# Kernel optimization log

Hardware: AMD Instinct MI355X
Metric: run time of the kernel (lower is better)

The kernel has to match this reference:

```python
import jax, jax.numpy as jnp
import numpy as np

DIM = 3072
HEADS = 24
HD = 128
FF = 4 * DIM
EPS = 1e-6
SCALE_SHIFT = 1.0


def _ln(x):
    # LayerNorm, elementwise_affine=False
    mu = jnp.mean(x, axis=-1, keepdims=True)
    var = jnp.mean(jnp.square(x - mu), axis=-1, keepdims=True)
    return (x - mu) * jax.lax.rsqrt(var + EPS)


def _rms(x, w):
    # RMSNorm over head_dim with learned weight
    ms = jnp.mean(jnp.square(x), axis=-1, keepdims=True)
    return x * jax.lax.rsqrt(ms + EPS) * w


def _rope(x, cos, sin):
    # x: [B,S,H,D], cos/sin: [S,D]; interleaved rotate-half (diffusers style)
    xr = x.reshape(*x.shape[:-1], -1, 2)
    x1, x2 = xr[..., 0], xr[..., 1]
    rot = jnp.stack([-x2, x1], axis=-1).reshape(x.shape)
    return x * cos[None, :, None, :] + rot * sin[None, :, None, :]


def _mod_params(temb, w, b):
    m = jax.nn.silu(temb) @ w + b  # [B, 6*DIM]
    B = m.shape[0]
    m = m.reshape(B, -1, 6).transpose(0, 2, 1).reshape(B, -1)  # reorder to 6 blocks of DIM
    return jnp.split(m, 2, axis=-1)  # mod1, mod2 each [B, 3*DIM]


def _modulate(x, mp):
    shift, scale, gate = jnp.split(mp, 3, axis=-1)
    scale = scale + SCALE_SHIFT
    return x * scale[:, None, :] + shift[:, None, :], gate[:, None, :]


def setup_inputs() -> dict:
    key = jax.random.key(0)
    ks = jax.random.split(key, 32)
    B, ST, SI = 1, 512, 1024
    S = ST + SI
    r = lambda k, shp, s=1.0: jax.random.normal(k, shp, dtype=jnp.float32) * s
    W = 0.02  # weight init scale
    ang = jax.random.uniform(ks[5], (S, HD), minval=0.0, maxval=2 * np.pi)
    inp = {
        "hidden_states": r(ks[0], (B, SI, DIM)),
        "encoder_hidden_states": r(ks[1], (B, ST, DIM)),
        "encoder_hidden_states_mask": jnp.ones((B, ST), jnp.float32),
        "temb": r(ks[2], (B, DIM)),
        "rope_cos": jnp.cos(ang),
        "rope_sin": jnp.sin(ang),
        "w_img_mod": r(ks[6], (DIM, 6 * DIM), W), "b_img_mod": r(ks[7], (6 * DIM,), W),
        "w_txt_mod": r(ks[8], (DIM, 6 * DIM), W), "b_txt_mod": r(ks[9], (6 * DIM,), W),
        "norm_q_w": jnp.ones((HD,), jnp.float32), "norm_k_w": jnp.ones((HD,), jnp.float32),
        "norm_added_q_w": jnp.ones((HD,), jnp.float32), "norm_added_k_w": jnp.ones((HD,), jnp.float32),
        "w_qkv": r(ks[10], (DIM, 3 * DIM), W), "b_qkv": r(ks[11], (3 * DIM,), W),
        "w_add_qkv": r(ks[12], (DIM, 3 * DIM), W), "b_add_qkv": r(ks[13], (3 * DIM,), W),
        "w_out": r(ks[14], (DIM, DIM), W), "b_out": r(ks[15], (DIM,), W),
        "w_add_out": r(ks[16], (DIM, DIM), W), "b_add_out": r(ks[17], (DIM,), W),
        "w_img_mlp1": r(ks[18], (DIM, FF), W), "b_img_mlp1": r(ks[19], (FF,), W),
        "w_img_mlp2": r(ks[20], (FF, DIM), W), "b_img_mlp2": r(ks[21], (DIM,), W),
        "w_txt_mlp1": r(ks[22], (DIM, FF), W), "b_txt_mlp1": r(ks[23], (FF,), W),
        "w_txt_mlp2": r(ks[24], (FF, DIM), W), "b_txt_mlp2": r(ks[25], (DIM,), W),
    }
    return inp


def reference(hidden_states, encoder_hidden_states, encoder_hidden_states_mask, temb,
              rope_cos, rope_sin,
              w_img_mod, b_img_mod, w_txt_mod, b_txt_mod,
              norm_q_w, norm_k_w, norm_added_q_w, norm_added_k_w,
              w_qkv, b_qkv, w_add_qkv, b_add_qkv,
              w_out, b_out, w_add_out, b_add_out,
              w_img_mlp1, b_img_mlp1, w_img_mlp2, b_img_mlp2,
              w_txt_mlp1, b_txt_mlp1, w_txt_mlp2, b_txt_mlp2):
    B, SI, _ = hidden_states.shape
    ST = encoder_hidden_states.shape[1]

    img_mod1, img_mod2 = _mod_params(temb, w_img_mod, b_img_mod)
    txt_mod1, txt_mod2 = _mod_params(temb, w_txt_mod, b_txt_mod)

    img_m, img_g1 = _modulate(_ln(hidden_states), img_mod1)
    txt_m, txt_g1 = _modulate(_ln(encoder_hidden_states), txt_mod1)

    # joint attention
    iq, ik, iv = jnp.split(img_m @ w_qkv + b_qkv, 3, axis=-1)
    tq, tk, tv = jnp.split(txt_m @ w_add_qkv + b_add_qkv, 3, axis=-1)
    iq = _rms(iq.reshape(B, SI, HEADS, HD), norm_q_w)
    ik = _rms(ik.reshape(B, SI, HEADS, HD), norm_k_w)
    iv = iv.reshape(B, SI, HEADS, HD)
    tq = _rms(tq.reshape(B, ST, HEADS, HD), norm_added_q_w)
    tk = _rms(tk.reshape(B, ST, HEADS, HD), norm_added_k_w)
    tv = tv.reshape(B, ST, HEADS, HD)
    q = jnp.concatenate([tq, iq], axis=1)  # [B,S,H,D], txt first
    k = jnp.concatenate([tk, ik], axis=1)
    v = jnp.concatenate([tv, iv], axis=1)
    q = _rope(q, rope_cos, rope_sin)
    k = _rope(k, rope_cos, rope_sin)
    scores = jnp.einsum('bqhd,bkhd->bhqk', q, k) / np.float32(np.sqrt(HD))
    probs = jax.nn.softmax(scores, axis=-1)
    attn = jnp.einsum('bhqk,bkhd->bqhd', probs, v).reshape(B, ST + SI, HEADS * HD)

    txt_a = attn[:, :ST] @ w_add_out + b_add_out
    img_a = attn[:, ST:] @ w_out + b_out
    hidden = hidden_states + img_g1 * img_a
    enc = encoder_hidden_states + txt_g1 * txt_a

    # fused GELU(tanh) MLPs with modulation
    img_m2, img_g2 = _modulate(_ln(hidden), img_mod2)
    img_mlp = jax.nn.gelu(img_m2 @ w_img_mlp1 + b_img_mlp1, approximate=True) @ w_img_mlp2 + b_img_mlp2
    hidden = hidden + img_g2 * img_mlp

    txt_m2, txt_g2 = _modulate(_ln(enc), txt_mod2)
    txt_mlp = jax.nn.gelu(txt_m2 @ w_txt_mlp1 + b_txt_mlp1, approximate=True) @ w_txt_mlp2 + b_txt_mlp2
    enc = enc + txt_g2 * txt_mlp

    return enc, hidden
```

## Files before the change

### kernel.cpp

```cpp
#include <hip/hip_runtime.h>

#define DIMX 3072
#define STX 512
#define SIX 1024
#define SQX 1536
#define FFX 12288

typedef __attribute__((ext_vector_type(4))) float f32x4;
typedef __attribute__((ext_vector_type(8))) __bf16 bf16x8;
typedef __attribute__((ext_vector_type(4))) int i32x4;

__device__ __forceinline__ unsigned short f2bf(float f){
  unsigned u = __builtin_bit_cast(unsigned, f);
  u += 0x7FFFu + ((u>>16)&1u);
  return (unsigned short)(u>>16);
}
__device__ __forceinline__ float bf2f(unsigned short h){
  unsigned u = ((unsigned)h)<<16;
  return __builtin_bit_cast(float, u);
}
__device__ __forceinline__ float gelu_tanh(float x){
  float x3 = x*x*x;
  float z = 0.7978845608028654f*(x + 0.044715f*x3);
  z = fminf(fmaxf(z, -15.f), 15.f);
  float e = exp2f(z*2.8853900817779268f);
  float th = (e-1.f)/(e+1.f);
  return 0.5f*x*(1.f+th);
}

__device__ __forceinline__ void gload16(const unsigned short* g, unsigned short* l){
  __builtin_amdgcn_global_load_lds(
      (const __attribute__((address_space(1))) void*)g,
      (__attribute__((address_space(3))) void*)l,
      16, 0, 0);
}


__global__ void k_silu(const float* __restrict__ temb, float* __restrict__ out){
  int i = blockIdx.x*256 + threadIdx.x;
  if(i < DIMX){
    float x = temb[i];
    out[i] = x / (1.f + exp2f(-x*1.4426950408889634f));
  }
}

__global__ void k_modinit(const float* __restrict__ b_img, const float* __restrict__ b_txt,
                          float* __restrict__ mod){
  int idx = blockIdx.x*256 + threadIdx.x;
  int mat = idx / 18432; int r = idx % 18432;
  int i = r/6, j = r%6;
  const float* b = mat ? b_txt : b_img;
  mod[mat*18432 + j*3072 + i] = b[r];
}

__global__ void k_modgemv(const float* __restrict__ w_img, const float* __restrict__ w_txt,
                          const float* __restrict__ silu_t, float* __restrict__ mod){
  int bz = blockIdx.x;
  int ks = bz & 7; bz >>= 3;
  int nc = bz % 18; int mat = bz / 18;
  const float* W = mat ? w_txt : w_img;
  __shared__ float st[384];
  int k0 = ks*384;
  for(int i = threadIdx.x; i < 384; i += 256) st[i] = silu_t[k0+i];
  __syncthreads();
  int n0 = nc*1024 + threadIdx.x*4;
  float ax=0.f, ay=0.f, az=0.f, aw=0.f;
  const float* Wp = W + (size_t)k0*18432 + n0;
  #pragma unroll 4
  for(int k=0;k<384;k++){
    float4 w = *(const float4*)(Wp + (size_t)k*18432);
    float s = st[k];
    ax += s*w.x; ay += s*w.y; az += s*w.z; aw += s*w.w;
  }
  float* md = mod + mat*18432;
  float vals[4] = {ax, ay, az, aw};
  #pragma unroll
  for(int j=0;j<4;j++){
    int n = n0+j; int i = n/6, jj = n%6;
    atomicAdd(&md[jj*3072 + i], vals[j]);
  }
}

__global__ void k_wconvT(const float* __restrict__ W, unsigned short* __restrict__ WT,
                         int Ktot, int Ntot){
  __shared__ float tile[64][65];
  int k0 = blockIdx.x*64, n0 = blockIdx.y*64;
  int t = threadIdx.x;
  {
    int r = t>>2;
    int cb = (t&3)*16;
    const float* src = W + (size_t)(k0+r)*Ntot + n0 + cb;
    #pragma unroll
    for(int j=0;j<4;j++){
      float4 v = *(const float4*)(src + 4*j);
      tile[r][cb+4*j+0] = v.x; tile[r][cb+4*j+1] = v.y;
      tile[r][cb+4*j+2] = v.z; tile[r][cb+4*j+3] = v.w;
    }
  }
  __syncthreads();
  {
    int n = t>>2;
    int kb = (t&3)*16;
    unsigned short* dst = WT + (size_t)(n0+n)*Ktot + k0 + kb;
    #pragma unroll
    for(int j2=0;j2<2;j2++){
      unsigned pk[4];
      #pragma unroll
      for(int p=0;p<4;p++){
        int k = kb + j2*8 + p*2;
        unsigned short a = f2bf(tile[k][n]);
        unsigned short b = f2bf(tile[k+1][n]);
        pk[p] = (unsigned)a | ((unsigned)b<<16);
      }
      i32x4 dv = {(int)pk[0],(int)pk[1],(int)pk[2],(int)pk[3]};
      *(i32x4*)(dst + j2*8) = dv;
    }
  }
}

__global__ void k_initC(float* __restrict__ out, const float* __restrict__ res,
                        const float* __restrict__ gate, const float* __restrict__ bias){
  int i = (blockIdx.x*256 + threadIdx.x)*4;
  int col = i % 3072;
  float4 r = *(const float4*)(res + i);
  float4 g = *(const float4*)(gate + col);
  float4 b = *(const float4*)(bias + col);
  float4 o = {r.x + g.x*b.x, r.y + g.y*b.y, r.z + g.z*b.z, r.w + g.w*b.w};
  *(float4*)(out + i) = o;
}

__global__ void k_f2b(const float* __restrict__ x, unsigned short* __restrict__ y, int n4){
  int i = blockIdx.x*256 + threadIdx.x;
  if(i < n4){
    float4 v = *(const float4*)(x + (size_t)i*4);
    unsigned short h0 = f2bf(v.x), h1 = f2bf(v.y), h2 = f2bf(v.z), h3 = f2bf(v.w);
    unsigned long long pk = (unsigned long long)(h0 | ((unsigned)h1<<16))
                          | ((unsigned long long)(h2 | ((unsigned)h3<<16))<<32);
    *(unsigned long long*)(y + (size_t)i*4) = pk;
  }
}

__global__ void k_lnmod(const float* __restrict__ x, const float* __restrict__ modp,
                        unsigned short* __restrict__ out){
  int row = blockIdx.x, t = threadIdx.x;
  const float* xr = x + (size_t)row*DIMX;
  float4 v0 = *(const float4*)(xr + t*4);
  float4 v1 = *(const float4*)(xr + 1024 + t*4);
  float4 v2 = *(const float4*)(xr + 2048 + t*4);
  float s  = v0.x+v0.y+v0.z+v0.w + v1.x+v1.y+v1.z+v1.w + v2.x+v2.y+v2.z+v2.w;
  float s2 = v0.x*v0.x+v0.y*v0.y+v0.z*v0.z+v0.w*v0.w
           + v1.x*v1.x+v1.y*v1.y+v1.z*v1.z+v1.w*v1.w
           + v2.x*v2.x+v2.y*v2.y+v2.z*v2.z+v2.w*v2.w;
  #pragma unroll
  for(int o=32;o>0;o>>=1){ s += __shfl_xor(s,o); s2 += __shfl_xor(s2,o); }
  __shared__ float rs_[4], rs2_[4];
  int wid = t>>6;
  if((t&63)==0){ rs_[wid]=s; rs2_[wid]=s2; }
  __syncthreads();
  float S  = rs_[0]+rs_[1]+rs_[2]+rs_[3];
  float S2 = rs2_[0]+rs2_[1]+rs2_[2]+rs2_[3];
  float mu = S*(1.f/3072.f);
  float var = S2*(1.f/3072.f) - mu*mu;
  float rstd = rsqrtf(var + 1e-6f);
  #pragma unroll
  for(int j=0;j<3;j++){
    int c = j*1024 + t*4;
    float4 sh = *(const float4*)(modp + c);
    float4 sc = *(const float4*)(modp + 3072 + c);
    float4 xv = (j==0)?v0:((j==1)?v1:v2);
    unsigned short h0 = f2bf((xv.x-mu)*rstd*(sc.x+1.f)+sh.x);
    unsigned short h1 = f2bf((xv.y-mu)*rstd*(sc.y+1.f)+sh.y);
    unsigned short h2 = f2bf((xv.z-mu)*rstd*(sc.z+1.f)+sh.z);
    unsigned short h3 = f2bf((xv.w-mu)*rstd*(sc.w+1.f)+sh.w);
    unsigned long long pk = (unsigned long long)(h0 | ((unsigned)h1<<16))
                          | ((unsigned long long)(h2 | ((unsigned)h3<<16))<<32);
    *(unsigned long long*)(out + (size_t)row*DIMX + c) = pk;
  }
}

__global__ void k_rmsrope(const unsigned short* __restrict__ qkv_txt,
                          const unsigned short* __restrict__ qkv_img,
                          const float* __restrict__ nqw, const float* __restrict__ nkw,
                          const float* __restrict__ naqw, const float* __restrict__ nakw,
                          const float* __restrict__ cosb, const float* __restrict__ sinb,
                          unsigned short* __restrict__ Q, unsigned short* __restrict__ K,
                          unsigned short* __restrict__ V){
  int s = blockIdx.x, h = blockIdx.y, t = threadIdx.x;
  bool txt = s < STX;
  const unsigned short* src = txt ? (qkv_txt + (size_t)s*9216)
                                  : (qkv_img + (size_t)(s-STX)*9216);
  const float* qw = txt ? naqw : nqw;
  const float* kw = txt ? nakw : nkw;
  int d0 = 2*t;
  float q1 = bf2f(src[h*128 + d0]),        q2 = bf2f(src[h*128 + d0 + 1]);
  float k1 = bf2f(src[3072 + h*128 + d0]), k2 = bf2f(src[3072 + h*128 + d0 + 1]);
  float v1 = bf2f(src[6144 + h*128 + d0]), v2 = bf2f(src[6144 + h*128 + d0 + 1]);
  float sq = q1*q1 + q2*q2, sk = k1*k1 + k2*k2;
  #pragma unroll
  for(int o=32;o>0;o>>=1){ sq += __shfl_xor(sq,o); sk += __shfl_xor(sk,o); }
  float rq = rsqrtf(sq*(1.f/128.f) + 1e-6f);
  float rk = rsqrtf(sk*(1.f/128.f) + 1e-6f);
  q1 *= rq*qw[d0]; q2 *= rq*qw[d0+1];
  k1 *= rk*kw[d0]; k2 *= rk*kw[d0+1];
  float c1 = cosb[(size_t)s*128 + d0], c2 = cosb[(size_t)s*128 + d0 + 1];
  float s1 = sinb[(size_t)s*128 + d0], s2 = sinb[(size_t)s*128 + d0 + 1];
  float Q1 = q1*c1 - q2*s1, Q2 = q2*c2 + q1*s2;
  float K1 = k1*c1 - k2*s1, K2 = k2*c2 + k1*s2;
  size_t o = ((size_t)s*24 + h)*128 + d0;
  Q[o] = f2bf(Q1); Q[o+1] = f2bf(Q2);
  K[o] = f2bf(K1); K[o+1] = f2bf(K2);
  V[o] = f2bf(v1); V[o+1] = f2bf(v2);
}

__global__ void k_vtrans(const unsigned short* __restrict__ V, unsigned short* __restrict__ VT){
  __shared__ unsigned short tile[64][136];
  int st = blockIdx.x, h = blockIdx.y, t = threadIdx.x;
  int s0 = st*64;
  {
    int s = t>>2;
    #pragma unroll
    for(int i=0;i<4;i++){
      int oct = ((t&3)<<2) + i;
      i32x4 d = *(const i32x4*)(V + ((size_t)(s0+s)*24 + h)*128 + oct*8);
      *(i32x4*)&tile[s][oct*8] = d;
    }
  }
  __syncthreads();
  {
    int d0 = t>>3; int strip = t&7;
    #pragma unroll
    for(int i=0;i<4;i++){
      int d = d0 + i*32;
      unsigned short h8[8];
      #pragma unroll
      for(int j=0;j<8;j++) h8[j] = tile[strip*8 + j][d];
      unsigned a0 = h8[0] | ((unsigned)h8[1]<<16);
      unsigned a1 = h8[2] | ((unsigned)h8[3]<<16);
      unsigned a2 = h8[4] | ((unsigned)h8[5]<<16);
      unsigned a3 = h8[6] | ((unsigned)h8[7]<<16);
      i32x4 dv = {(int)a0,(int)a1,(int)a2,(int)a3};
      *(i32x4*)(VT + ((size_t)h*128 + d)*1536 + s0 + strip*8) = dv;
    }
  }
}

__global__ void k_softmax(unsigned short* __restrict__ S){
  size_t row = blockIdx.x;
  unsigned short* p = S + row*1536;
  int t = threadIdx.x;
  float v[6];
  float m = -1e30f;
  #pragma unroll
  for(int j=0;j<6;j++){ v[j] = bf2f(p[t + j*256]); m = fmaxf(m, v[j]); }
  #pragma unroll
  for(int o=32;o>0;o>>=1) m = fmaxf(m, __shfl_xor(m, o));
  __shared__ float red[4];
  int wid = t>>6;
  if((t&63)==0) red[wid] = m;
  __syncthreads();
  float M = fmaxf(fmaxf(red[0],red[1]), fmaxf(red[2],red[3]));
  __syncthreads();
  float s = 0.f;
  #pragma unroll
  for(int j=0;j<6;j++){ v[j] = exp2f((v[j]-M)*1.4426950408889634f); s += v[j]; }
  #pragma unroll
  for(int o=32;o>0;o>>=1) s += __shfl_xor(s, o);
  if((t&63)==0) red[wid] = s;
  __syncthreads();
  float inv = 1.f/(red[0]+red[1]+red[2]+red[3]);
  #pragma unroll
  for(int j=0;j<6;j++) p[t + j*256] = f2bf(v[j]*inv);
}

__global__ __launch_bounds__(256,4) void k_gemm(
    const unsigned short* __restrict__ A, long lda, long sAz,
    const unsigned short* __restrict__ BT, long ldb, long sBz,
    const float* __restrict__ bias,
    void* __restrict__ Cp, long ldc, long sCz,
    int K, int KS, int mode, float alpha,
    const float* __restrict__ gate)
{
  __shared__ unsigned short Als[128*32];
  __shared__ unsigned short Bls[128*32];
  const int t = threadIdx.x;
  const int bn = blockIdx.x, bm = blockIdx.y;
  const int z = blockIdx.z, zh = z / KS, zs = z - zh*KS;
  const int Kc = K / KS, kbeg = zs*Kc, kend = kbeg + Kc;

  const unsigned short* Ab = A  + (size_t)zh*sAz + (size_t)bm*128*lda;
  const unsigned short* Bb = BT + (size_t)zh*sBz + (size_t)bn*128*ldb;

  const int lane = t & 63, wid = t>>6, wr = wid>>1, wc = wid&1;
  const int lr = lane & 15, lk = lane>>4;

  const int srow = (lane>>2);
  const int soff = (lane&3)*8;

  f32x4 acc[4][4];
  #pragma unroll
  for(int i=0;i<4;i++)
    #pragma unroll
    for(int j=0;j<4;j++) acc[i][j] = {0.f,0.f,0.f,0.f};

  for(int k0=kbeg; k0<kend; k0+=32){
    __syncthreads();
    gload16(Ab + (size_t)(     wid*16 + srow)*lda + k0 + soff, Als + (     wid*16)*32);
    gload16(Ab + (size_t)(64 + wid*16 + srow)*lda + k0 + soff, Als + (64 + wid*16)*32);
    gload16(Bb + (size_t)(     wid*16 + srow)*ldb + k0 + soff, Bls + (     wid*16)*32);
    gload16(Bb + (size_t)(64 + wid*16 + srow)*ldb + k0 + soff, Bls + (64 + wid*16)*32);
    __syncthreads();
    bf16x8 af[4], bfr[4];
    #pragma unroll
    for(int mf=0;mf<4;mf++) af[mf]  = *(const bf16x8*)&Als[(wr*64 + mf*16 + lr)*32 + lk*8];
    #pragma unroll
    for(int nf=0;nf<4;nf++) bfr[nf] = *(const bf16x8*)&Bls[(wc*64 + nf*16 + lr)*32 + lk*8];
    #pragma unroll
    for(int mf=0;mf<4;mf++)
      #pragma unroll
      for(int nf=0;nf<4;nf++)
        acc[mf][nf] = __builtin_amdgcn_mfma_f32_16x16x32_bf16(af[mf], bfr[nf], acc[mf][nf], 0,0,0);
  }

  unsigned short* C16 = (unsigned short*)Cp + (size_t)zh*sCz;
  float* C32 = (float*)Cp + (size_t)zh*sCz;
  #pragma unroll
  for(int mf=0;mf<4;mf++){
    #pragma unroll
    for(int nf=0;nf<4;nf++){
      #pragma unroll
      for(int r=0;r<4;r++){
        size_t row = (size_t)bm*128 + wr*64 + mf*16 + lk*4 + r;
        size_t col = (size_t)bn*128 + wc*64 + nf*16 + lr;
        float v = acc[mf][nf][r]*alpha;
        if(mode==0){
          C16[row*ldc + col] = f2bf(v + (bias ? bias[col] : 0.f));
        } else if(mode==1){
          C16[row*ldc + col] = f2bf(gelu_tanh(v + (bias ? bias[col] : 0.f)));
        } else {
          float g = gate ? gate[col] : 1.f;
          atomicAdd(&C32[row*ldc + col], g*v);
        }
      }
    }
  }
}


extern "C" void kernel_launch(void* const* d_in, const int* in_sizes, int n_in,
                              void* d_out, int out_size, void* d_ws, size_t ws_size,
                              hipStream_t stream){
  const float* hidden_states = (const float*)d_in[0];
  const float* enc_states    = (const float*)d_in[1];
  const float* temb          = (const float*)d_in[3];
  const float* rope_cos      = (const float*)d_in[4];
  const float* rope_sin      = (const float*)d_in[5];
  const float* w_img_mod     = (const float*)d_in[6];
  const float* b_img_mod     = (const float*)d_in[7];
  const float* w_txt_mod     = (const float*)d_in[8];
  const float* b_txt_mod     = (const float*)d_in[9];
  const float* norm_q_w      = (const float*)d_in[10];
  const float* norm_k_w      = (const float*)d_in[11];
  const float* norm_aq_w     = (const float*)d_in[12];
  const float* norm_ak_w     = (const float*)d_in[13];
  const float* w_qkv   = (const float*)d_in[14];
  const float* b_qkv   = (const float*)d_in[15];
  const float* w_aqkv  = (const float*)d_in[16];
  const float* b_aqkv  = (const float*)d_in[17];
  const float* w_out_  = (const float*)d_in[18];
  const float* b_out_  = (const float*)d_in[19];
  const float* w_aout  = (const float*)d_in[20];
  const float* b_aout  = (const float*)d_in[21];
  const float* w_mlp1i = (const float*)d_in[22];
  const float* b_mlp1i = (const float*)d_in[23];
  const float* w_mlp2i = (const float*)d_in[24];
  const float* b_mlp2i = (const float*)d_in[25];
  const float* w_mlp1t = (const float*)d_in[26];
  const float* b_mlp1t = (const float*)d_in[27];
  const float* w_mlp2t = (const float*)d_in[28];
  const float* b_mlp2t = (const float*)d_in[29];

  char* ws = (char*)d_ws;
  float* mod    = (float*)(ws + 0);
  float* silu_t = (float*)(ws + 147456);
  unsigned short* imgm = (unsigned short*)(ws + 159744);
  unsigned short* txtm = (unsigned short*)(ws + 6451200);
  float* hid = (float*)(ws + 9596928);
  float* enc = (float*)(ws + 22179840);
  float* attnf = (float*)(ws + 28471296);
  unsigned short* Qb  = (unsigned short*)(ws + 47345664);
  unsigned short* Kb  = (unsigned short*)(ws + 56782848);
  unsigned short* Vb  = (unsigned short*)(ws + 66220032);
  unsigned short* attnb = (unsigned short*)(ws + 66220032);
  unsigned short* VTb = (unsigned short*)(ws + 75657216);
  unsigned short* WT1  = (unsigned short*)(ws + 85094400);
  unsigned short* WT1b = (unsigned short*)(ws + 85094400 + 18874368);
  unsigned short* Sbuf = (unsigned short*)(ws + 85094400);
  unsigned short* qkvi = (unsigned short*)(ws + 141717504);
  unsigned short* qkvt = (unsigned short*)(ws + 160591872);
  unsigned short* WTm  = (unsigned short*)(ws + 28471296);
  unsigned short* mlph = (unsigned short*)(ws + 103968768);

  float* out_enc = (float*)d_out;
  float* out_hid = (float*)d_out + (size_t)STX*DIMX;

  k_silu<<<12,256,0,stream>>>(temb, silu_t);
  k_modinit<<<144,256,0,stream>>>(b_img_mod, b_txt_mod, mod);
  k_modgemv<<<288,256,0,stream>>>(w_img_mod, w_txt_mod, silu_t, mod);

  k_lnmod<<<SIX,256,0,stream>>>(hidden_states, mod + 0,     imgm);
  k_lnmod<<<STX,256,0,stream>>>(enc_states,    mod + 18432, txtm);

  k_wconvT<<<dim3(48,144),256,0,stream>>>(w_qkv, WT1, 3072, 9216);
  k_gemm<<<dim3(72,8,1),256,0,stream>>>(imgm,3072,0, WT1,3072,0, b_qkv,
      qkvi,9216,0, 3072,1, 0, 1.f, nullptr);
  k_wconvT<<<dim3(48,144),256,0,stream>>>(w_aqkv, WT1, 3072, 9216);
  k_gemm<<<dim3(72,4,1),256,0,stream>>>(txtm,3072,0, WT1,3072,0, b_aqkv,
      qkvt,9216,0, 3072,1, 0, 1.f, nullptr);

  k_rmsrope<<<dim3(1536,24),64,0,stream>>>(qkvt, qkvi, norm_q_w, norm_k_w,
      norm_aq_w, norm_ak_w, rope_cos, rope_sin, Qb, Kb, Vb);
  k_vtrans<<<dim3(24,24),256,0,stream>>>(Vb, VTb);

  hipMemsetAsync(attnf, 0, (size_t)1536*3072*4, stream);
  for(int g=0; g<3; g++){
    long hb = g*8;
    k_gemm<<<dim3(12,12,8),256,0,stream>>>(Qb + hb*128, 3072, 128,
        Kb + hb*128, 3072, 128, nullptr,
        Sbuf, 1536, (long)1536*1536, 128,1, 0, 0.08838834764831845f, nullptr);
    k_softmax<<<8*1536,256,0,stream>>>(Sbuf);
    k_gemm<<<dim3(1,12,32),256,0,stream>>>(Sbuf, 1536, (long)1536*1536,
        VTb + (size_t)hb*128*1536, 1536, (long)128*1536, nullptr,
        attnf + hb*128, 3072, 128, 1536,4, 3, 1.f, nullptr);
  }
  k_f2b<<<4608,256,0,stream>>>(attnf, attnb, 1536*3072/4);

  k_wconvT<<<dim3(48,48),256,0,stream>>>(w_aout, WT1, 3072, 3072);
  k_wconvT<<<dim3(48,48),256,0,stream>>>(w_out_, WT1b, 3072, 3072);
  k_initC<<<512*3,256,0,stream>>>(enc, enc_states, mod + 18432 + 2*3072, b_aout);
  k_initC<<<1024*3,256,0,stream>>>(hid, hidden_states, mod + 2*3072, b_out_);
  k_gemm<<<dim3(24,4,4),256,0,stream>>>(attnb,3072,0, WT1,3072,0, nullptr,
      enc,3072,0, 3072,4, 3, 1.f, mod + 18432 + 2*3072);
  k_gemm<<<dim3(24,8,4),256,0,stream>>>(attnb + (size_t)512*3072,3072,0, WT1b,3072,0, nullptr,
      hid,3072,0, 3072,4, 3, 1.f, mod + 2*3072);

  k_lnmod<<<SIX,256,0,stream>>>(hid, mod + 3*3072, imgm);
  k_wconvT<<<dim3(48,192),256,0,stream>>>(w_mlp1i, WTm, 3072, 12288);
  k_gemm<<<dim3(96,8,1),256,0,stream>>>(imgm,3072,0, WTm,3072,0, b_mlp1i,
      mlph,12288,0, 3072,1, 1, 1.f, nullptr);
  k_wconvT<<<dim3(192,48),256,0,stream>>>(w_mlp2i, WTm, 12288, 3072);
  k_initC<<<1024*3,256,0,stream>>>(out_hid, hid, mod + 5*3072, b_mlp2i);
  k_gemm<<<dim3(24,8,4),256,0,stream>>>(mlph,12288,0, WTm,12288,0, nullptr,
      out_hid,3072,0, 12288,4, 3, 1.f, mod + 5*3072);

  k_lnmod<<<STX,256,0,stream>>>(enc, mod + 18432 + 3*3072, txtm);
  k_wconvT<<<dim3(48,192),256,0,stream>>>(w_mlp1t, WTm, 3072, 12288);
  k_gemm<<<dim3(96,4,1),256,0,stream>>>(txtm,3072,0, WTm,3072,0, b_mlp1t,
      mlph,12288,0, 3072,1, 1, 1.f, nullptr);
  k_wconvT<<<dim3(192,48),256,0,stream>>>(w_mlp2t, WTm, 12288, 3072);
  k_initC<<<512*3,256,0,stream>>>(out_enc, enc, mod + 18432 + 5*3072, b_mlp2t);
  k_gemm<<<dim3(24,4,8),256,0,stream>>>(mlph,12288,0, WTm,12288,0, nullptr,
      out_enc,3072,0, 12288,8, 3, 1.f, mod + 18432 + 5*3072);
}
```

Before: 1.345 ms.

## Fuse fp32 weight conversion into GEMM, reading fp32 weights directly

Drops the separate transpose-and-convert-to-bf16 pass over every weight matrix. A new GEMM variant streams the fp32 weight tiles straight into LDS and converts them to bf16 while building the MFMA B fragments. This saves a full read and write of each weight through HBM. In exchange the GEMM loads twice as many weight bytes per tile, does strided LDS reads with likely bank conflicts, and runs conversion work in the inner loop. The weight tiles are re-read and re-converted by every M-block.

```diff
diff --git a/kernel.cpp b/kernel.cpp
--- a/kernel.cpp
+++ b/kernel.cpp
@@ -28,7 +28,7 @@
   return 0.5f*x*(1.f+th);
 }
 
-__device__ __forceinline__ void gload16(const unsigned short* g, unsigned short* l){
+__device__ __forceinline__ void gload16(const void* g, void* l){
   __builtin_amdgcn_global_load_lds(
       (const __attribute__((address_space(1))) void*)g,
       (__attribute__((address_space(3))) void*)l,
@@ -78,43 +78,6 @@
   for(int j=0;j<4;j++){
     int n = n0+j; int i = n/6, jj = n%6;
     atomicAdd(&md[jj*3072 + i], vals[j]);
-  }
-}
-
-__global__ void k_wconvT(const float* __restrict__ W, unsigned short* __restrict__ WT,
-                         int Ktot, int Ntot){
-  __shared__ float tile[64][65];
-  int k0 = blockIdx.x*64, n0 = blockIdx.y*64;
-  int t = threadIdx.x;
-  {
-    int r = t>>2;
-    int cb = (t&3)*16;
-    const float* src = W + (size_t)(k0+r)*Ntot + n0 + cb;
-    #pragma unroll
-    for(int j=0;j<4;j++){
-      float4 v = *(const float4*)(src + 4*j);
-      tile[r][cb+4*j+0] = v.x; tile[r][cb+4*j+1] = v.y;
-      tile[r][cb+4*j+2] = v.z; tile[r][cb+4*j+3] = v.w;
-    }
-  }
-  __syncthreads();
-  {
-    int n = t>>2;
-    int kb = (t&3)*16;
-    unsigned short* dst = WT + (size_t)(n0+n)*Ktot + k0 + kb;
-    #pragma unroll
-    for(int j2=0;j2<2;j2++){
-      unsigned pk[4];
-      #pragma unroll
-      for(int p=0;p<4;p++){
-        int k = kb + j2*8 + p*2;
-        unsigned short a = f2bf(tile[k][n]);
-        unsigned short b = f2bf(tile[k+1][n]);
-        pk[p] = (unsigned)a | ((unsigned)b<<16);
-      }
-      i32x4 dv = {(int)pk[0],(int)pk[1],(int)pk[2],(int)pk[3]};
-      *(i32x4*)(dst + j2*8) = dv;
-    }
   }
 }
 
@@ -292,7 +255,6 @@
 
   const int lane = t & 63, wid = t>>6, wr = wid>>1, wc = wid&1;
   const int lr = lane & 15, lk = lane>>4;
-
   const int srow = (lane>>2);
   const int soff = (lane&3)*8;
 
@@ -332,6 +294,89 @@
         size_t row = (size_t)bm*128 + wr*64 + mf*16 + lk*4 + r;
         size_t col = (size_t)bn*128 + wc*64 + nf*16 + lr;
         float v = acc[mf][nf][r]*alpha;
+        if(mode==0){
+          C16[row*ldc + col] = f2bf(v + (bias ? bias[col] : 0.f));
+        } else if(mode==1){
+          C16[row*ldc + col] = f2bf(gelu_tanh(v + (bias ? bias[col] : 0.f)));
+        } else {
+          float g = gate ? gate[col] : 1.f;
+          atomicAdd(&C32[row*ldc + col], g*v);
+        }
+      }
+    }
+  }
+}
+
+__global__ __launch_bounds__(256,4) void k_gemmW(
+    const unsigned short* __restrict__ A, long lda,
+    const float* __restrict__ W, long ldw,
+    const float* __restrict__ bias,
+    void* __restrict__ Cp, long ldc,
+    int K, int KS, int mode,
+    const float* __restrict__ gate)
+{
+  __shared__ unsigned short Als[128*32];
+  __shared__ float BlsW[32*128];
+  const int t = threadIdx.x;
+  const int bn = blockIdx.x, bm = blockIdx.y;
+  const int zs = blockIdx.z;
+  const int Kc = K / KS, kbeg = zs*Kc, kend = kbeg + Kc;
+
+  const unsigned short* Ab = A + (size_t)bm*128*lda;
+  const float* Wb = W + (size_t)bn*128;
+
+  const int lane = t & 63, wid = t>>6, wr = wid>>1, wc = wid&1;
+  const int lr = lane & 15, lk = lane>>4;
+  const int srow = (lane>>2);
+  const int soff = (lane&3)*8;
+  const int wrow = (lane>>5);
+  const int wcol = (lane&31)*4;
+
+  f32x4 acc[4][4];
+  #pragma unroll
+  for(int i=0;i<4;i++)
+    #pragma unroll
+    for(int j=0;j<4;j++) acc[i][j] = {0.f,0.f,0.f,0.f};
+
+  for(int k0=kbeg; k0<kend; k0+=32){
+    __syncthreads();
+    gload16(Ab + (size_t)(     wid*16 + srow)*lda + k0 + soff, Als + (     wid*16)*32);
+    gload16(Ab + (size_t)(64 + wid*16 + srow)*lda + k0 + soff, Als + (64 + wid*16)*32);
+    #pragma unroll
+    for(int i=0;i<4;i++){
+      int r0 = wid*8 + i*2;
+      gload16(Wb + (size_t)(k0 + r0 + wrow)*ldw + wcol, BlsW + r0*128);
+    }
+    __syncthreads();
+    bf16x8 af[4], bfr[4];
+    #pragma unroll
+    for(int mf=0;mf<4;mf++) af[mf] = *(const bf16x8*)&Als[(wr*64 + mf*16 + lr)*32 + lk*8];
+    #pragma unroll
+    for(int nf=0;nf<4;nf++){
+      const float* Bcol = BlsW + lk*8*128 + wc*64 + nf*16 + lr;
+      bf16x8 bv;
+      #pragma unroll
+      for(int j=0;j<8;j++) bv[j] = (__bf16)Bcol[j*128];
+      bfr[nf] = bv;
+    }
+    #pragma unroll
+    for(int mf=0;mf<4;mf++)
+      #pragma unroll
+      for(int nf=0;nf<4;nf++)
+        acc[mf][nf] = __builtin_amdgcn_mfma_f32_16x16x32_bf16(af[mf], bfr[nf], acc[mf][nf], 0,0,0);
+  }
+
+  unsigned short* C16 = (unsigned short*)Cp;
+  float* C32 = (float*)Cp;
+  #pragma unroll
+  for(int mf=0;mf<4;mf++){
+    #pragma unroll
+    for(int nf=0;nf<4;nf++){
+      #pragma unroll
+      for(int r=0;r<4;r++){
+        size_t row = (size_t)bm*128 + wr*64 + mf*16 + lk*4 + r;
+        size_t col = (size_t)bn*128 + wc*64 + nf*16 + lr;
+        float v = acc[mf][nf][r];
         if(mode==0){
           C16[row*ldc + col] = f2bf(v + (bias ? bias[col] : 0.f));
         } else if(mode==1){
@@ -392,12 +437,9 @@
   unsigned short* Vb  = (unsigned short*)(ws + 66220032);
   unsigned short* attnb = (unsigned short*)(ws + 66220032);
   unsigned short* VTb = (unsigned short*)(ws + 75657216);
-  unsigned short* WT1  = (unsigned short*)(ws + 85094400);
-  unsigned short* WT1b = (unsigned short*)(ws + 85094400 + 18874368);
   unsigned short* Sbuf = (unsigned short*)(ws + 85094400);
   unsigned short* qkvi = (unsigned short*)(ws + 141717504);
   unsigned short* qkvt = (unsigned short*)(ws + 160591872);
-  unsigned short* WTm  = (unsigned short*)(ws + 28471296);
   unsigned short* mlph = (unsigned short*)(ws + 103968768);
 
   float* out_enc = (float*)d_out;
@@ -410,12 +452,10 @@
   k_lnmod<<<SIX,256,0,stream>>>(hidden_states, mod + 0,     imgm);
   k_lnmod<<<STX,256,0,stream>>>(enc_states,    mod + 18432, txtm);
 
-  k_wconvT<<<dim3(48,144),256,0,stream>>>(w_qkv, WT1, 3072, 9216);
-  k_gemm<<<dim3(72,8,1),256,0,stream>>>(imgm,3072,0, WT1,3072,0, b_qkv,
-      qkvi,9216,0, 3072,1, 0, 1.f, nullptr);
-  k_wconvT<<<dim3(48,144),256,0,stream>>>(w_aqkv, WT1, 3072, 9216);
-  k_gemm<<<dim3(72,4,1),256,0,stream>>>(txtm,3072,0, WT1,3072,0, b_aqkv,
-      qkvt,9216,0, 3072,1, 0, 1.f, nullptr);
+  k_gemmW<<<dim3(72,8,1),256,0,stream>>>(imgm,3072, w_qkv,9216, b_qkv,
+      qkvi,9216, 3072,1, 0, nullptr);
+  k_gemmW<<<dim3(72,4,1),256,0,stream>>>(txtm,3072, w_aqkv,9216, b_aqkv,
+      qkvt,9216, 3072,1, 0, nullptr);
 
   k_rmsrope<<<dim3(1536,24),64,0,stream>>>(qkvt, qkvi, norm_q_w, norm_k_w,
       norm_aq_w, norm_ak_w, rope_cos, rope_sin, Qb, Kb, Vb);
@@ -434,30 +474,24 @@
   }
   k_f2b<<<4608,256,0,stream>>>(attnf, attnb, 1536*3072/4);
 
-  k_wconvT<<<dim3(48,48),256,0,stream>>>(w_aout, WT1, 3072, 3072);
-  k_wconvT<<<dim3(48,48),256,0,stream>>>(w_out_, WT1b, 3072, 3072);
   k_initC<<<512*3,256,0,stream>>>(enc, enc_states, mod + 18432 + 2*3072, b_aout);
   k_initC<<<1024*3,256,0,stream>>>(hid, hidden_states, mod + 2*3072, b_out_);
-  k_gemm<<<dim3(24,4,4),256,0,stream>>>(attnb,3072,0, WT1,3072,0, nullptr,
-      enc,3072,0, 3072,4, 3, 1.f, mod + 18432 + 2*3072);
-  k_gemm<<<dim3(24,8,4),256,0,stream>>>(attnb + (size_t)512*3072,3072,0, WT1b,3072,0, nullptr,
-      hid,3072,0, 3072,4, 3, 1.f, mod + 2*3072);
+  k_gemmW<<<dim3(24,4,4),256,0,stream>>>(attnb,3072, w_aout,3072, nullptr,
+      enc,3072, 3072,4, 3, mod + 18432 + 2*3072);
+  k_gemmW<<<dim3(24,8,4),256,0,stream>>>(attnb + (size_t)512*3072,3072, w_out_,3072, nullptr,
+      hid,3072, 3072,4, 3, mod + 2*3072);
 
   k_lnmod<<<SIX,256,0,stream>>>(hid, mod + 3*3072, imgm);
-  k_wconvT<<<dim3(48,192),256,0,stream>>>(w_mlp1i, WTm, 3072, 12288);
-  k_gemm<<<dim3(96,8,1),256,0,stream>>>(imgm,3072,0, WTm,3072,0, b_mlp1i,
-      mlph,12288,0, 3072,1, 1, 1.f, nullptr);
-  k_wconvT<<<dim3(192,48),256,0,stream>>>(w_mlp2i, WTm, 12288, 3072);
+  k_gemmW<<<dim3(96,8,1),256,0,stream>>>(imgm,3072, w_mlp1i,12288, b_mlp1i,
+      mlph,12288, 3072,1, 1, nullptr);
   k_initC<<<1024*3,256,0,stream>>>(out_hid, hid, mod + 5*3072, b_mlp2i);
-  k_gemm<<<dim3(24,8,4),256,0,stream>>>(mlph,12288,0, WTm,12288,0, nullptr,
-      out_hid,3072,0, 12288,4, 3, 1.f, mod + 5*3072);
+  k_gemmW<<<dim3(24,8,4),256,0,stream>>>(mlph,12288, w_mlp2i,3072, nullptr,
+      out_hid,3072, 12288,4, 3, mod + 5*3072);
 
   k_lnmod<<<STX,256,0,stream>>>(enc, mod + 18432 + 3*3072, txtm);
-  k_wconvT<<<dim3(48,192),256,0,stream>>>(w_mlp1t, WTm, 3072, 12288);
-  k_gemm<<<dim3(96,4,1),256,0,stream>>>(txtm,3072,0, WTm,3072,0, b_mlp1t,
-      mlph,12288,0, 3072,1, 1, 1.f, nullptr);
-  k_wconvT<<<dim3(192,48),256,0,stream>>>(w_mlp2t, WTm, 12288, 3072);
+  k_gemmW<<<dim3(96,4,1),256,0,stream>>>(txtm,3072, w_mlp1t,12288, b_mlp1t,
+      mlph,12288, 3072,1, 1, nullptr);
   k_initC<<<512*3,256,0,stream>>>(out_enc, enc, mod + 18432 + 5*3072, b_mlp2t);
-  k_gemm<<<dim3(24,4,8),256,0,stream>>>(mlph,12288,0, WTm,12288,0, nullptr,
-      out_enc,3072,0, 12288,8, 3, 1.f, mod + 18432 + 5*3072);
-}
+  k_gemmW<<<dim3(24,4,8),256,0,stream>>>(mlph,12288, w_mlp2t,3072, nullptr,
+      out_enc,3072, 12288,8, 3, mod + 18432 + 5*3072);
+}
```

Result: no change. 1.372 ms (+2.0%).
